# Kernel tuning notes

Measured on AMD Instinct MI355X. Metric: run time of the kernel, lower is better.

The kernel has to match this reference:

```python
import jax, jax.numpy as jnp
import numpy as np

# Skeleton structure (start, end) connections
REAL_CONNECTIONS = [(0,1),(1,2),(2,3),(3,4),(1,5),(5,6),(6,7),(7,8),(8,9),(8,13),(8,17),(8,21),(8,25),(9,10),(10,11),(11,12),(13,14),(14,15),(15,16),(17,18),(18,19),(19,20),(21,22),(22,23),(23,24),(25,26),(26,27),(27,28),(4,29),(29,30),(29,34),(29,38),(29,42),(29,46),(30,31),(31,32),(32,33),(34,35),(35,36),(36,37),(38,39),(39,40),(40,41),(42,43),(43,44),(44,45),(46,47),(47,48),(48,49)]

def _bone_ranges():
    # dict insertion order matters only for iteration; result is a sum so order-free
    ranges = {(0,1):(0.05,0.15),(1,2):(0.1,0.2),(1,5):(0.1,0.2),(2,3):(0.2,0.35),(3,4):(0.2,0.35),(5,6):(0.2,0.35),(6,7):(0.2,0.35),(4,8):(0.05,0.15),(7,29):(0.05,0.15)}
    for s, e in REAL_CONNECTIONS:
        if 8 <= s < 50 and 8 <= e < 50:
            ranges[(s, e)] = (0.01, 0.08)
    return ranges

_BR = _bone_ranges()
BONE_S = np.array([k[0] for k in _BR], np.int32)
BONE_E = np.array([k[1] for k in _BR], np.int32)
BONE_MIN = np.array([v[0] for v in _BR.values()], np.float32)
BONE_MAX = np.array([v[1] for v in _BR.values()], np.float32)

SYM_L = np.array([8 + i for i in range(21)] + [2, 3, 4], np.int32)
SYM_R = np.array([29 + i for i in range(21)] + [5, 6, 7], np.int32)

ANG_A = np.array([1, 1, 2, 5], np.int32)
ANG_B = np.array([2, 5, 3, 6], np.int32)
ANG_C = np.array([3, 6, 4, 7], np.int32)

CONN_S = np.array([c[0] for c in REAL_CONNECTIONS], np.int32)
CONN_E = np.array([c[1] for c in REAL_CONNECTIONS], np.int32)

DEG = np.float32(180.0 / np.pi)
EPS = np.float32(1e-12)

def _relu(x):
    return jnp.maximum(x, 0.0)

def _normalize(v):
    n = jnp.linalg.norm(v, axis=-1, keepdims=True)
    return v / jnp.maximum(n, EPS)

def setup_inputs() -> dict:
    key = jax.random.key(0)
    k1, k2 = jax.random.split(key)
    B, S, D = 64, 2048, 150
    pred_poses = jax.random.normal(k1, (B, S, D), dtype=jnp.float32)
    target_poses = jax.random.normal(k2, (B, S, D), dtype=jnp.float32)
    return {"pred_poses": pred_poses, "target_poses": target_poses}

def reference(pred_poses, target_poses):
    B, S, _ = pred_poses.shape
    J = pred_poses.reshape(B, S, 50, 3)
    T = target_poses.reshape(B, S, 50, 3)

    # ---- bone length loss (49 constrained bones, one gathered pass) ----
    bv = J[:, :, BONE_E] - J[:, :, BONE_S]                 # [B,S,49,3]
    bl = jnp.linalg.norm(bv, axis=-1)                      # [B,S,49]
    bone_pen = _relu(bl - BONE_MAX) + _relu(BONE_MIN - bl)
    bone_loss = bone_pen.mean()  # == sum over bones of per-bone mean / n_bones

    # ---- joint angle loss (4 triples) ----
    v1 = _normalize(J[:, :, ANG_A] - J[:, :, ANG_B])       # [B,S,4,3]
    v2 = _normalize(J[:, :, ANG_C] - J[:, :, ANG_B])
    cos = jnp.clip(jnp.sum(v1 * v2, axis=-1), -1.0, 1.0)
    deg = jnp.arccos(cos) * DEG
    angle_loss = (_relu(30.0 - deg) + _relu(deg - 150.0)).mean()

    # ---- symmetry loss (24 pairs) ----
    L = J[:, :, SYM_L]                                     # [B,S,24,3]
    R = J[:, :, SYM_R]
    x_sym = jnp.abs(L[..., 0] + R[..., 0])                 # [B,S,24]
    yz_sim = jnp.abs(L[..., 1:] - R[..., 1:]).mean(axis=-1)
    symmetry_loss = (x_sym + yz_sim).mean()

    # ---- temporal consistency ----
    vel = J[:, 1:] - J[:, :-1]                             # [B,S-1,50,3]
    acc = vel[:, 1:] - vel[:, :-1]
    temporal_loss = jnp.linalg.norm(acc, axis=-1).mean() + 0.5 * jnp.linalg.norm(vel, axis=-1).mean()

    # ---- supervised bone-length consistency (all 49 connections) ----
    tb = jnp.linalg.norm(T[:, :, CONN_E] - T[:, :, CONN_S], axis=-1)
    pb = jnp.linalg.norm(J[:, :, CONN_E] - J[:, :, CONN_S], axis=-1)
    supervised_loss = jnp.abs(pb - tb).mean()

    total = (1.0 * bone_loss + 0.5 * angle_loss + 0.3 * symmetry_loss
             + 0.2 * temporal_loss + supervised_loss)
    return bone_loss, angle_loss, symmetry_loss, temporal_loss, supervised_loss, total
```

## Files before the change

### kernel.cpp

```cpp
#include <hip/hip_runtime.h>
#include <math.h>

#define TPB 512
#define CH  16
#define CPB 8

static constexpr int B_     = 64;
static constexpr int S_     = 2048;
static constexpr int TOTAL  = B_ * S_;
static constexpr int NCHUNK = TOTAL / CH;
static constexpr int NBLK   = NCHUNK / CPB;
static constexpr int SAMPB  = 600;
static constexpr int PREDB  = (CH + 2) * SAMPB;
static constexpr int TGTB   = CH * SAMPB;
static constexpr int CHB    = PREDB + TGTB;
static constexpr int BUFB   = 20480;
static constexpr long TOTB  = (long)TOTAL * SAMPB;

__constant__ int US_[51] = {0,1,1,2,3,5,6,4,7,7,4,
    8,8,8,8,8,9,10,11,13,14,
    15,17,18,19,21,22,23,25,26,27,
    29,29,29,29,29,30,31,32,34,35,
    36,38,39,40,42,43,44,46,47,48};
__constant__ int UE_[51] = {1,2,5,3,4,6,7,8,29,8,29,
    9,13,17,21,25,10,11,12,14,15,
    16,18,19,20,22,23,24,26,27,28,
    30,34,38,42,46,31,32,33,35,36,
    37,39,40,41,43,44,45,47,48,49};
__constant__ float UMIN11_[11] = {0.05f,0.1f,0.1f,0.2f,0.2f,0.2f,0.2f,0.05f,0.05f,-1e9f,-1e9f};
__constant__ float UMAX11_[11] = {0.15f,0.2f,0.2f,0.35f,0.35f,0.35f,0.35f,0.15f,0.15f,1e9f,1e9f};
__constant__ float WSUP11_[11] = {1.f,1.f,1.f,1.f,1.f,1.f,1.f,0.f,0.f,1.f,1.f};
__constant__ int SL_[24] = {8,9,10,11,12,13,14,15,16,17,18,19,20,21,22,23,24,25,26,27,28,2,3,4};
__constant__ int SR_[24] = {29,30,31,32,33,34,35,36,37,38,39,40,41,42,43,44,45,46,47,48,49,5,6,7};
__constant__ int AJ_[4] = {1,1,2,5};
__constant__ int BJ_[4] = {2,5,3,6};
__constant__ int CJ_[4] = {3,6,4,7};

struct F3 { float x, y, z; };
__device__ __forceinline__ F3 ld3(const float* p) { return *(const F3*)p; }

typedef const __attribute__((address_space(1))) void* gas_t;
typedef __attribute__((address_space(3))) void* las_t;

__global__ __launch_bounds__(TPB, 8) void pose_main(
    const float* __restrict__ pred, const float* __restrict__ tgt,
    float* __restrict__ part)
{
    __shared__ __align__(16) char LDS[2 * BUFB];

    const int tid = threadIdx.x;
    const int blk = blockIdx.x;
    const int li  = tid & 15;
    const int g   = tid >> 4;
    const int jb  = li * 150;

    const int   uS0 = jb + US_[g] * 3, uE0 = jb + UE_[g] * 3;
    const float uMn0 = (g < 11) ? UMIN11_[g] : 0.01f;
    const float uMx0 = (g < 11) ? UMAX11_[g] : 0.08f;
    const float uW0  = (g < 11) ? WSUP11_[g] : 1.f;
    const bool u1_on = (g < 19);
    const int  k1u   = u1_on ? g + 32 : 50;
    const int  uS1 = jb + US_[k1u] * 3, uE1 = jb + UE_[k1u] * 3;
    const bool sy_on = (g < 24);
    const int  ks  = sy_on ? g : 0;
    const int  s0L = jb + SL_[ks] * 3, s0R = jb + SR_[ks] * 3;
    const int aA = jb + AJ_[g & 3] * 3, aB = jb + BJ_[g & 3] * 3, aC = jb + CJ_[g & 3] * 3;
    const int  tb0 = jb + 3 * g;
    const bool t1_on = (g < 18);

    float a_bone = 0.f, a_ang = 0.f, a_sym = 0.f, a_vel = 0.f, a_acc = 0.f, a_sup = 0.f;

    const int w      = tid >> 6;
    const int lane16 = (tid & 63) << 4;
    auto stage = [&](int cidx, char* lbuf) {
        const long nb = (long)cidx * TGTB;
        const char* pb = (const char*)pred + nb;
        const char* tb = (const char*)tgt  + nb - PREDB;
        const long prem = TOTB - nb - 16;
        #pragma unroll
        for (int s = 0; s < 3; ++s) {
            const int slice = w + s * 8;
            if (slice < 20) {
                const long o = (long)slice * 1024 + lane16;
                const char* src = (o < PREDB)
                    ? pb + (o > prem ? prem : o)
                    : tb + (o > (long)(CHB - 16) ? (long)(CHB - 16) : o);
                __builtin_amdgcn_global_load_lds((gas_t)src, (las_t)(lbuf + slice * 1024), 16, 0, 0);
            }
        }
    };

    const int c0 = blk * CPB;
    stage(c0, LDS);

    #pragma unroll
    for (int c = 0; c < CPB; ++c) {
        char* curb = LDS + (c & 1) * BUFB;
        char* nxtb = LDS + ((c & 1) ^ 1) * BUFB;
        if (c + 1 < CPB) {
            stage(c0 + c + 1, nxtb);
            if (tid < 256) asm volatile("s_waitcnt vmcnt(3)" ::: "memory");
            else           asm volatile("s_waitcnt vmcnt(2)" ::: "memory");
        } else {
            asm volatile("s_waitcnt vmcnt(0)" ::: "memory");
        }
        __builtin_amdgcn_s_barrier();
        __builtin_amdgcn_sched_barrier(0);

        const float* Jl = (const float*)curb;
        const float* Tl = Jl + PREDB / 4;
        const int cidx = c0 + c;

        {
            const F3 je = ld3(Jl + uE0), js = ld3(Jl + uS0);
            const float dx = je.x - js.x, dy = je.y - js.y, dz = je.z - js.z;
            const float pb = sqrtf(dx * dx + dy * dy + dz * dz);
            a_bone += fmaxf(pb - uMx0, 0.f) + fmaxf(uMn0 - pb, 0.f);
            const F3 te = ld3(Tl + uE0), ts = ld3(Tl + uS0);
            const float tx = te.x - ts.x, ty = te.y - ts.y, tz = te.z - ts.z;
            const float tb = sqrtf(tx * tx + ty * ty + tz * tz);
            a_sup += uW0 * fabsf(pb - tb);
        }
        if (u1_on) {
            const F3 je = ld3(Jl + uE1), js = ld3(Jl + uS1);
            const float dx = je.x - js.x, dy = je.y - js.y, dz = je.z - js.z;
            const float pb = sqrtf(dx * dx + dy * dy + dz * dz);
            a_bone += fmaxf(pb - 0.08f, 0.f) + fmaxf(0.01f - pb, 0.f);
            const F3 te = ld3(Tl + uE1), ts = ld3(Tl + uS1);
            const float tx = te.x - ts.x, ty = te.y - ts.y, tz = te.z - ts.z;
            const float tb = sqrtf(tx * tx + ty * ty + tz * tz);
            a_sup += fabsf(pb - tb);
        }

        if (sy_on) {
            const F3 L = ld3(Jl + s0L), R = ld3(Jl + s0R);
            a_sym += fabsf(L.x + R.x) + 0.5f * (fabsf(L.y - R.y) + fabsf(L.z - R.z));
        }

        if (tid < 64) {
            const F3 A = ld3(Jl + aA), Bb = ld3(Jl + aB), C = ld3(Jl + aC);
            const float v1x = A.x - Bb.x, v1y = A.y - Bb.y, v1z = A.z - Bb.z;
            const float v2x = C.x - Bb.x, v2y = C.y - Bb.y, v2z = C.z - Bb.z;
            const float n12 = (v1x*v1x + v1y*v1y + v1z*v1z) * (v2x*v2x + v2y*v2y + v2z*v2z);
            const float inv = __frsqrt_rn(fmaxf(n12, 1e-24f));
            float cosv = (v1x*v2x + v1y*v2y + v1z*v2z) * inv;
            cosv = fminf(fmaxf(cosv, -1.f), 1.f);
            const float deg = acosf(cosv) * 57.29577951308232f;
            a_ang += fmaxf(30.f - deg, 0.f) + fmaxf(deg - 150.f, 0.f);
        }

        {
            const int sidx = ((cidx * CH) & (S_ - 1)) + li;
            const bool v_ok = sidx < S_ - 1;
            const bool a_ok = sidx < S_ - 2;
            {
                const float* tp = Jl + tb0;
                const F3 p0 = ld3(tp), p1 = ld3(tp + 150), p2 = ld3(tp + 300);
                if (v_ok) {
                    const float vx = p1.x - p0.x, vy = p1.y - p0.y, vz = p1.z - p0.z;
                    a_vel += sqrtf(vx*vx + vy*vy + vz*vz);
                    if (a_ok) {
                        const float ax = p2.x - 2.f*p1.x + p0.x;
                        const float ay = p2.y - 2.f*p1.y + p0.y;
                        const float az = p2.z - 2.f*p1.z + p0.z;
                        a_acc += sqrtf(ax*ax + ay*ay + az*az);
                    }
                }
            }
            if (t1_on) {
                const float* tq = Jl + tb0 + 96;
                const F3 p0 = ld3(tq), p1 = ld3(tq + 150), p2 = ld3(tq + 300);
                if (v_ok) {
                    const float vx = p1.x - p0.x, vy = p1.y - p0.y, vz = p1.z - p0.z;
                    a_vel += sqrtf(vx*vx + vy*vy + vz*vz);
                    if (a_ok) {
                        const float ax = p2.x - 2.f*p1.x + p0.x;
                        const float ay = p2.y - 2.f*p1.y + p0.y;
                        const float az = p2.z - 2.f*p1.z + p0.z;
                        a_acc += sqrtf(ax*ax + ay*ay + az*az);
                    }
                }
            }
        }

        asm volatile("" ::: "memory");
        __builtin_amdgcn_s_barrier();
    }

    float vals[6] = {a_bone, a_ang, a_sym, a_vel, a_acc, a_sup};
    #pragma unroll
    for (int k = 0; k < 6; ++k)
        #pragma unroll
        for (int off = 32; off > 0; off >>= 1)
            vals[k] += __shfl_down(vals[k], off, 64);

    float* red = (float*)LDS;
    const int lane = tid & 63;
    if (lane == 0) {
        #pragma unroll
        for (int k = 0; k < 6; ++k) red[w * 6 + k] = vals[k];
    }
    __syncthreads();
    if (tid == 0) {
        #pragma unroll
        for (int k = 0; k < 6; ++k) {
            float s = 0.f;
            #pragma unroll
            for (int v = 0; v < 8; ++v) s += red[v * 6 + k];
            part[k * NBLK + blk] = s;
        }
    }
}

__global__ __launch_bounds__(256) void pose_reduce(
    const float* __restrict__ part, float* __restrict__ out)
{
    __shared__ float red[4][6];
    const int tid = threadIdx.x;
    float a[6];
    #pragma unroll
    for (int k = 0; k < 6; ++k) {
        float s = 0.f;
        for (int i = tid; i < NBLK; i += 256) s += part[k * NBLK + i];
        a[k] = s;
    }
    #pragma unroll
    for (int k = 0; k < 6; ++k)
        #pragma unroll
        for (int off = 32; off > 0; off >>= 1)
            a[k] += __shfl_down(a[k], off, 64);

    const int wid = tid >> 6, lane = tid & 63;
    if (lane == 0) {
        #pragma unroll
        for (int k = 0; k < 6; ++k) red[wid][k] = a[k];
    }
    __syncthreads();
    if (tid == 0) {
        float t[6];
        #pragma unroll
        for (int k = 0; k < 6; ++k) t[k] = red[0][k] + red[1][k] + red[2][k] + red[3][k];
        const float bone = t[0] * (1.f / ((float)TOTAL * 49.f));
        const float ang  = t[1] * (1.f / ((float)TOTAL * 4.f));
        const float sym  = t[2] * (1.f / ((float)TOTAL * 24.f));
        const float temporal = t[4] * (1.f / ((float)B_ * (float)(S_ - 2) * 50.f))
                             + 0.5f * t[3] * (1.f / ((float)B_ * (float)(S_ - 1) * 50.f));
        const float sup  = t[5] * (1.f / ((float)TOTAL * 49.f));
        out[0] = bone;
        out[1] = ang;
        out[2] = sym;
        out[3] = temporal;
        out[4] = sup;
        out[5] = bone + 0.5f * ang + 0.3f * sym + 0.2f * temporal + sup;
    }
}

extern "C" void kernel_launch(void* const* d_in, const int* in_sizes, int n_in,
                              void* d_out, int out_size, void* d_ws, size_t ws_size,
                              hipStream_t stream)
{
    const float* pred = (const float*)d_in[0];
    const float* tgt  = (const float*)d_in[1];
    float* part = (float*)d_ws;
    pose_main<<<NBLK, TPB, 0, stream>>>(pred, tgt, part);
    pose_reduce<<<1, 256, 0, stream>>>(part, (float*)d_out);
}
```

Before: 44.06 us.

## Double chunk size to 32 samples per stage and remap thread work

Result: faster. 39.27 us (-10.9%).

```diff
diff --git a/kernel.cpp b/kernel.cpp
--- a/kernel.cpp
+++ b/kernel.cpp
@@ -2,7 +2,7 @@
 #include <math.h>
 
 #define TPB 512
-#define CH  16
+#define CH  32
 #define CPB 8
 
 static constexpr int B_     = 64;
@@ -14,7 +14,8 @@
 static constexpr int PREDB  = (CH + 2) * SAMPB;
 static constexpr int TGTB   = CH * SAMPB;
 static constexpr int CHB    = PREDB + TGTB;
-static constexpr int BUFB   = 20480;
+static constexpr int NSLICE = 39;
+static constexpr int BUFB   = NSLICE * 1024;
 static constexpr long TOTB  = (long)TOTAL * SAMPB;
 
 __constant__ int US_[51] = {0,1,1,2,3,5,6,4,7,7,4,
@@ -38,11 +39,12 @@
 
 struct F3 { float x, y, z; };
 __device__ __forceinline__ F3 ld3(const float* p) { return *(const F3*)p; }
+#define SQRTF __builtin_amdgcn_sqrtf
 
 typedef const __attribute__((address_space(1))) void* gas_t;
 typedef __attribute__((address_space(3))) void* las_t;
 
-__global__ __launch_bounds__(TPB, 8) void pose_main(
+__global__ __launch_bounds__(TPB, 4) void pose_main(
     const float* __restrict__ pred, const float* __restrict__ tgt,
     float* __restrict__ part)
 {
@@ -50,23 +52,24 @@
 
     const int tid = threadIdx.x;
     const int blk = blockIdx.x;
-    const int li  = tid & 15;
-    const int g   = tid >> 4;
+    const int li  = tid & 31;
+    const int g   = tid >> 5;
     const int jb  = li * 150;
 
-    const int   uS0 = jb + US_[g] * 3, uE0 = jb + UE_[g] * 3;
+    const int   uS0 = jb + US_[g] * 3,      uE0 = jb + UE_[g] * 3;
     const float uMn0 = (g < 11) ? UMIN11_[g] : 0.01f;
     const float uMx0 = (g < 11) ? UMAX11_[g] : 0.08f;
     const float uW0  = (g < 11) ? WSUP11_[g] : 1.f;
-    const bool u1_on = (g < 19);
-    const int  k1u   = u1_on ? g + 32 : 50;
-    const int  uS1 = jb + US_[k1u] * 3, uE1 = jb + UE_[k1u] * 3;
-    const bool sy_on = (g < 24);
-    const int  ks  = sy_on ? g : 0;
-    const int  s0L = jb + SL_[ks] * 3, s0R = jb + SR_[ks] * 3;
+    const int   uS1 = jb + US_[g + 16] * 3, uE1 = jb + UE_[g + 16] * 3;
+    const int   uS2 = jb + US_[g + 32] * 3, uE2 = jb + UE_[g + 32] * 3;
+    const int   kx  = 48 + (g < 3 ? g : 0);
+    const int   uSx = jb + US_[kx] * 3,     uEx = jb + UE_[kx] * 3;
+    const int s0L = jb + SL_[g] * 3,           s0R = jb + SR_[g] * 3;
+    const int s1L = jb + SL_[16 + (g & 7)] * 3, s1R = jb + SR_[16 + (g & 7)] * 3;
     const int aA = jb + AJ_[g & 3] * 3, aB = jb + BJ_[g & 3] * 3, aC = jb + CJ_[g & 3] * 3;
-    const int  tb0 = jb + 3 * g;
-    const bool t1_on = (g < 18);
+    const int tb0 = jb + 3 * g;
+    const int tbx = jb + 144 + ((g - 4) & 1) * 3;
+    const bool tex_on = (g == 4 || g == 5);
 
     float a_bone = 0.f, a_ang = 0.f, a_sym = 0.f, a_vel = 0.f, a_acc = 0.f, a_sup = 0.f;
 
@@ -78,9 +81,9 @@
         const char* tb = (const char*)tgt  + nb - PREDB;
         const long prem = TOTB - nb - 16;
         #pragma unroll
-        for (int s = 0; s < 3; ++s) {
+        for (int s = 0; s < 5; ++s) {
             const int slice = w + s * 8;
-            if (slice < 20) {
+            if (slice < NSLICE) {
                 const long o = (long)slice * 1024 + lane16;
                 const char* src = (o < PREDB)
                     ? pb + (o > prem ? prem : o)
@@ -99,8 +102,8 @@
         char* nxtb = LDS + ((c & 1) ^ 1) * BUFB;
         if (c + 1 < CPB) {
             stage(c0 + c + 1, nxtb);
-            if (tid < 256) asm volatile("s_waitcnt vmcnt(3)" ::: "memory");
-            else           asm volatile("s_waitcnt vmcnt(2)" ::: "memory");
+            if (w < 7) asm volatile("s_waitcnt vmcnt(5)" ::: "memory");
+            else       asm volatile("s_waitcnt vmcnt(4)" ::: "memory");
         } else {
             asm volatile("s_waitcnt vmcnt(0)" ::: "memory");
         }
@@ -111,33 +114,29 @@
         const float* Tl = Jl + PREDB / 4;
         const int cidx = c0 + c;
 
-        {
-            const F3 je = ld3(Jl + uE0), js = ld3(Jl + uS0);
+        auto edge = [&](int so, int eo, float mn, float mx, float wsup) {
+            const F3 je = ld3(Jl + eo), js = ld3(Jl + so);
             const float dx = je.x - js.x, dy = je.y - js.y, dz = je.z - js.z;
-            const float pb = sqrtf(dx * dx + dy * dy + dz * dz);
-            a_bone += fmaxf(pb - uMx0, 0.f) + fmaxf(uMn0 - pb, 0.f);
-            const F3 te = ld3(Tl + uE0), ts = ld3(Tl + uS0);
+            const float pb = SQRTF(dx * dx + dy * dy + dz * dz);
+            a_bone += fmaxf(pb - mx, 0.f) + fmaxf(mn - pb, 0.f);
+            const F3 te = ld3(Tl + eo), ts = ld3(Tl + so);
             const float tx = te.x - ts.x, ty = te.y - ts.y, tz = te.z - ts.z;
-            const float tb = sqrtf(tx * tx + ty * ty + tz * tz);
-            a_sup += uW0 * fabsf(pb - tb);
-        }
-        if (u1_on) {
-            const F3 je = ld3(Jl + uE1), js = ld3(Jl + uS1);
-            const float dx = je.x - js.x, dy = je.y - js.y, dz = je.z - js.z;
-            const float pb = sqrtf(dx * dx + dy * dy + dz * dz);
-            a_bone += fmaxf(pb - 0.08f, 0.f) + fmaxf(0.01f - pb, 0.f);
-            const F3 te = ld3(Tl + uE1), ts = ld3(Tl + uS1);
-            const float tx = te.x - ts.x, ty = te.y - ts.y, tz = te.z - ts.z;
-            const float tb = sqrtf(tx * tx + ty * ty + tz * tz);
-            a_sup += fabsf(pb - tb);
-        }
-
-        if (sy_on) {
-            const F3 L = ld3(Jl + s0L), R = ld3(Jl + s0R);
+            const float tb = SQRTF(tx * tx + ty * ty + tz * tz);
+            a_sup += wsup * fabsf(pb - tb);
+        };
+        edge(uS0, uE0, uMn0, uMx0, uW0);
+        edge(uS1, uE1, 0.01f, 0.08f, 1.f);
+        edge(uS2, uE2, 0.01f, 0.08f, 1.f);
+        if (g < 3) edge(uSx, uEx, 0.01f, 0.08f, 1.f);
+
+        auto sym = [&](int l3, int r3) {
+            const F3 L = ld3(Jl + l3), R = ld3(Jl + r3);
             a_sym += fabsf(L.x + R.x) + 0.5f * (fabsf(L.y - R.y) + fabsf(L.z - R.z));
-        }
-
-        if (tid < 64) {
+        };
+        sym(s0L, s0R);
+        if (g < 8) sym(s1L, s1R);
+
+        if (g < 4) {
             const F3 A = ld3(Jl + aA), Bb = ld3(Jl + aB), C = ld3(Jl + aC);
             const float v1x = A.x - Bb.x, v1y = A.y - Bb.y, v1z = A.z - Bb.z;
             const float v2x = C.x - Bb.x, v2y = C.y - Bb.y, v2z = C.z - Bb.z;
@@ -153,34 +152,23 @@
             const int sidx = ((cidx * CH) & (S_ - 1)) + li;
             const bool v_ok = sidx < S_ - 1;
             const bool a_ok = sidx < S_ - 2;
-            {
-                const float* tp = Jl + tb0;
-                const F3 p0 = ld3(tp), p1 = ld3(tp + 150), p2 = ld3(tp + 300);
+            auto temporal = [&](int base) {
+                const F3 p0 = ld3(Jl + base), p1 = ld3(Jl + base + 150), p2 = ld3(Jl + base + 300);
                 if (v_ok) {
                     const float vx = p1.x - p0.x, vy = p1.y - p0.y, vz = p1.z - p0.z;
-                    a_vel += sqrtf(vx*vx + vy*vy + vz*vz);
+                    a_vel += SQRTF(vx*vx + vy*vy + vz*vz);
                     if (a_ok) {
                         const float ax = p2.x - 2.f*p1.x + p0.x;
                         const float ay = p2.y - 2.f*p1.y + p0.y;
                         const float az = p2.z - 2.f*p1.z + p0.z;
-                        a_acc += sqrtf(ax*ax + ay*ay + az*az);
+                        a_acc += SQRTF(ax*ax + ay*ay + az*az);
                     }
                 }
-            }
-            if (t1_on) {
-                const float* tq = Jl + tb0 + 96;
-                const F3 p0 = ld3(tq), p1 = ld3(tq + 150), p2 = ld3(tq + 300);
-                if (v_ok) {
-                    const float vx = p1.x - p0.x, vy = p1.y - p0.y, vz = p1.z - p0.z;
-                    a_vel += sqrtf(vx*vx + vy*vy + vz*vz);
-                    if (a_ok) {
-                        const float ax = p2.x - 2.f*p1.x + p0.x;
-                        const float ay = p2.y - 2.f*p1.y + p0.y;
-                        const float az = p2.z - 2.f*p1.z + p0.z;
-                        a_acc += sqrtf(ax*ax + ay*ay + az*az);
-                    }
-                }
-            }
+            };
+            temporal(tb0);
+            temporal(tb0 + 48);
+            temporal(tb0 + 96);
+            if (tex_on) temporal(tbx);
         }
 
         asm volatile("" ::: "memory");
```
